# Kernel optimization log

Hardware: AMD Instinct MI355X
Metric: run time of the kernel (lower is better)

Reference implementation:

```python
import jax, jax.numpy as jnp
import numpy as np

NUM_SAMPLE = 10


def setup_inputs() -> dict:
    key = jax.random.key(0)
    k1, k2, k3, k4, k5 = jax.random.split(key, 5)
    N, F, B, S = 100000, 256, 20000, NUM_SAMPLE
    features_ue = jax.random.normal(k1, (N, F), dtype=jnp.float32)
    features_ap = jax.random.normal(k2, (N, F), dtype=jnp.float32)
    neigh_idx = jax.random.randint(k3, (B, S), 0, N, dtype=jnp.int32)
    nodes = jax.random.randint(k4, (B,), 0, N, dtype=jnp.int32)
    # xavier-uniform weight [embed_dim, feature_dim] = [256, 2*F]
    embed_dim, feature_dim = 256, 2 * F
    limit = float(np.sqrt(6.0 / (embed_dim + feature_dim)))
    weight = jax.random.uniform(k5, (embed_dim, feature_dim), dtype=jnp.float32,
                                minval=-limit, maxval=limit)
    return {"features_ue": features_ue, "features_ap": features_ap,
            "neigh_idx": neigh_idx, "nodes": nodes, "weight": weight}


def reference(features_ue, features_ap, neigh_idx, nodes, weight):
    # sample_model='ue2ue': other_feature = self_feature = features_ue
    S = neigh_idx.shape[1]
    # gather sampled neighbor features: [B, S, F] -> sum over S
    gathered = jnp.take(features_ue, neigh_idx, axis=0)
    # original: mask.div(num_neigh + 1), i.e. divide by count PLUS one
    neigh_feats = gathered.sum(axis=1) / jnp.float32(S + 1)  # [B, F]
    self_feats = jnp.take(features_ue, nodes, axis=0)        # [B, F]
    combined = jnp.concatenate([self_feats, neigh_feats], axis=1)  # [B, 2F]
    # weight.mm(combined.t()) then relu -> [embed_dim, B]
    out = jax.nn.relu(jnp.einsum('ef,bf->eb', weight, combined))
    return out
```

## Files before the change

kernel.cpp:

```cpp
#include <hip/hip_runtime.h>

typedef __attribute__((ext_vector_type(8))) short short8;
typedef __attribute__((ext_vector_type(4))) float f32x4;

#define B_TOTAL 20000
#define B_PAD   20096
#define NF      256
#define K2      512
#define NS      10

__device__ __forceinline__ unsigned short f2bf(float x) {
    unsigned u = __builtin_bit_cast(unsigned, x);
    u += 0x7FFFu + ((u >> 16) & 1u);
    return (unsigned short)(u >> 16);
}

__global__ __launch_bounds__(256) void gather_combine(
    const float* __restrict__ ue, const int* __restrict__ nidx,
    const int* __restrict__ nodes, const float* __restrict__ w,
    unsigned short* __restrict__ comb, unsigned short* __restrict__ wbf)
{
    const int t = threadIdx.x, blk = blockIdx.x;
    if (blk < 128) {
        const int base = blk * 1024 + t * 4;
        const float4 v = *(const float4*)(w + base);
        ushort4 o;
        o.x = f2bf(v.x); o.y = f2bf(v.y); o.z = f2bf(v.z); o.w = f2bf(v.w);
        *(ushort4*)(wbf + base) = o;
    }
    const int lane = t & 63;
    const int b = blk * 4 + (t >> 6);
    if (b >= B_PAD) return;
    unsigned short* crow = comb + (size_t)b * K2;
    if (b < B_TOTAL) {
        const int node = nodes[b];
        const float4 sf = ((const float4*)(ue + (size_t)node * NF))[lane];
        int myidx = 0;
        if (lane < NS) myidx = nidx[b * NS + lane];
        float ax = 0.f, ay = 0.f, az = 0.f, aw = 0.f;
        #pragma unroll
        for (int s = 0; s < NS; ++s) {
            const int is = __shfl(myidx, s);
            const float4 v = ((const float4*)(ue + (size_t)is * NF))[lane];
            ax += v.x; ay += v.y; az += v.z; aw += v.w;
        }
        const float inv = 1.0f / 11.0f;
        ushort4 s4, n4;
        s4.x = f2bf(sf.x); s4.y = f2bf(sf.y); s4.z = f2bf(sf.z); s4.w = f2bf(sf.w);
        n4.x = f2bf(ax * inv); n4.y = f2bf(ay * inv);
        n4.z = f2bf(az * inv); n4.w = f2bf(aw * inv);
        *(ushort4*)(crow + lane * 4) = s4;
        *(ushort4*)(crow + NF + lane * 4) = n4;
    } else {
        ushort4 z; z.x = z.y = z.z = z.w = 0;
        *(ushort4*)(crow + lane * 4) = z;
        *(ushort4*)(crow + NF + lane * 4) = z;
    }
}

__global__ __launch_bounds__(256) void gemm_relu(
    const unsigned short* __restrict__ wbf,
    const unsigned short* __restrict__ comb,
    float* __restrict__ out)
{
    __shared__ unsigned short Alds[8192];
    __shared__ unsigned short Blds[2048];
    const int t    = threadIdx.x;
    const int lane = t & 63;
    const int wv   = t >> 6;
    const int n0   = blockIdx.x * 32;
    const int m0   = blockIdx.y * 128;
    const int fr   = lane & 15;
    const int kq   = lane >> 4;

    f32x4 acc[2][2] = {};
    const short8* A8 = (const short8*)Alds;
    const short8* B8 = (const short8*)Blds;

    for (int ks = 0; ks < 8; ++ks) {
        #pragma unroll
        for (int L = 0; L < 4; ++L) {
            const int d16 = L * 256 + t;
            const int g = d16 >> 7, row = d16 & 127;
            const unsigned short* src = wbf + (size_t)(m0 + row) * K2 + ks * 64 + g * 8;
            __builtin_amdgcn_global_load_lds(
                (const __attribute__((address_space(1))) void*)src,
                (__attribute__((address_space(3))) void*)(Alds + (size_t)d16 * 8), 16, 0, 0);
        }
        {
            const int g = t >> 5, row = t & 31;
            const unsigned short* src = comb + (size_t)(n0 + row) * K2 + ks * 64 + g * 8;
            __builtin_amdgcn_global_load_lds(
                (const __attribute__((address_space(1))) void*)src,
                (__attribute__((address_space(3))) void*)(Blds + (size_t)t * 8), 16, 0, 0);
        }
        asm volatile("s_waitcnt vmcnt(0)" ::: "memory");
        __syncthreads();

        #pragma unroll
        for (int h = 0; h < 2; ++h) {
            short8 af[2], bg[2];
            #pragma unroll
            for (int i = 0; i < 2; ++i)
                af[i] = A8[(h * 4 + kq) * 128 + wv * 32 + i * 16 + fr];
            #pragma unroll
            for (int j = 0; j < 2; ++j)
                bg[j] = B8[(h * 4 + kq) * 32 + j * 16 + fr];
            #pragma unroll
            for (int i = 0; i < 2; ++i)
                #pragma unroll
                for (int j = 0; j < 2; ++j)
                    acc[i][j] = __builtin_amdgcn_mfma_f32_16x16x32_bf16(af[i], bg[j], acc[i][j], 0, 0, 0);
        }
        __syncthreads();
    }

    #pragma unroll
    for (int i = 0; i < 2; ++i) {
        const int e = m0 + wv * 32 + i * 16 + kq * 4;
        #pragma unroll
        for (int j = 0; j < 2; ++j) {
            const int b = n0 + j * 16 + fr;
            if (b < B_TOTAL) {
                #pragma unroll
                for (int r = 0; r < 4; ++r)
                    out[(size_t)(e + r) * B_TOTAL + b] = fmaxf(acc[i][j][r], 0.0f);
            }
        }
    }
}

extern "C" void kernel_launch(void* const* d_in, const int* in_sizes, int n_in,
                              void* d_out, int out_size, void* d_ws, size_t ws_size,
                              hipStream_t stream) {
    const float* ue    = (const float*)d_in[0];
    const int*   nidx  = (const int*)d_in[2];
    const int*   nodes = (const int*)d_in[3];
    const float* w     = (const float*)d_in[4];
    float*       out   = (float*)d_out;

    unsigned short* comb = (unsigned short*)d_ws;
    unsigned short* wbf  = comb + (size_t)B_PAD * K2;

    hipLaunchKernelGGL(gather_combine, dim3(B_PAD / 4), dim3(256), 0, stream,
                       ue, nidx, nodes, w, comb, wbf);
    hipLaunchKernelGGL(gemm_relu, dim3(B_PAD / 32, 2), dim3(256), 0, stream,
                       wbf, comb, out);
}
```

Before: 68.16 us.

## Double-buffer GEMM LDS tiles and widen N tile to 64

Restructures the bf16 MFMA GEMM so global-to-LDS loads for the next K-slice (now 32 wide) are issued while the current slice is being computed, using two LDS buffers. The per-block N tile grows from 32 to 64, so each block does 2x4 MFMA tiles per wave and half as many blocks launch. The goal is to hide load latency and reuse the weight tile across more columns. The explicit vmcnt wait is dropped, so correctness now relies on the compiler inserting the wait before the barrier. The gather kernel, which likely dominates runtime, is unchanged.

```diff
diff --git a/kernel.cpp b/kernel.cpp
--- a/kernel.cpp
+++ b/kernel.cpp
@@ -63,63 +63,74 @@
     const unsigned short* __restrict__ comb,
     float* __restrict__ out)
 {
-    __shared__ unsigned short Alds[8192];
-    __shared__ unsigned short Blds[2048];
+    __shared__ unsigned short Alds[2][4096];
+    __shared__ unsigned short Blds[2][2048];
     const int t    = threadIdx.x;
     const int lane = t & 63;
     const int wv   = t >> 6;
-    const int n0   = blockIdx.x * 32;
+    const int n0   = blockIdx.x * 64;
     const int m0   = blockIdx.y * 128;
     const int fr   = lane & 15;
     const int kq   = lane >> 4;
 
-    f32x4 acc[2][2] = {};
-    const short8* A8 = (const short8*)Alds;
-    const short8* B8 = (const short8*)Blds;
+    const int arow = t & 127, akg = t >> 7;
+    const int brow = t & 63,  bkg = t >> 6;
 
-    for (int ks = 0; ks < 8; ++ks) {
+    const unsigned short* gaBase = wbf  + (size_t)(m0 + arow) * K2 + akg * 8;
+    const unsigned short* gbBase = comb + (size_t)(n0 + brow) * K2 + bkg * 8;
+
+#define STAGE(nb, ks)                                                            \
+    do {                                                                         \
+        const unsigned short* ga = gaBase + (ks) * 32;                           \
+        const unsigned short* gb = gbBase + (ks) * 32;                           \
+        __builtin_amdgcn_global_load_lds(                                        \
+            (const __attribute__((address_space(1))) void*)ga,                   \
+            (__attribute__((address_space(3))) void*)(&Alds[nb][0] + t * 8),     \
+            16, 0, 0);                                                           \
+        __builtin_amdgcn_global_load_lds(                                        \
+            (const __attribute__((address_space(1))) void*)(ga + 16),            \
+            (__attribute__((address_space(3))) void*)(&Alds[nb][2048] + t * 8),  \
+            16, 0, 0);                                                           \
+        __builtin_amdgcn_global_load_lds(                                        \
+            (const __attribute__((address_space(1))) void*)gb,                   \
+            (__attribute__((address_space(3))) void*)(&Blds[nb][0] + t * 8),     \
+            16, 0, 0);                                                           \
+    } while (0)
+
+    f32x4 acc[2][4] = {};
+
+    STAGE(0, 0);
+    __syncthreads();
+
+    #pragma unroll
+    for (int ks = 0; ks < 16; ++ks) {
+        const int cur = ks & 1;
+        if (ks < 15) STAGE(cur ^ 1, ks + 1);
+
+        const short8* A8 = (const short8*)Alds[cur];
+        const short8* B8 = (const short8*)Blds[cur];
+        short8 af[2], bg[4];
         #pragma unroll
-        for (int L = 0; L < 4; ++L) {
-            const int d16 = L * 256 + t;
-            const int g = d16 >> 7, row = d16 & 127;
-            const unsigned short* src = wbf + (size_t)(m0 + row) * K2 + ks * 64 + g * 8;
-            __builtin_amdgcn_global_load_lds(
-                (const __attribute__((address_space(1))) void*)src,
-                (__attribute__((address_space(3))) void*)(Alds + (size_t)d16 * 8), 16, 0, 0);
-        }
-        {
-            const int g = t >> 5, row = t & 31;
-            const unsigned short* src = comb + (size_t)(n0 + row) * K2 + ks * 64 + g * 8;
-            __builtin_amdgcn_global_load_lds(
-                (const __attribute__((address_space(1))) void*)src,
-                (__attribute__((address_space(3))) void*)(Blds + (size_t)t * 8), 16, 0, 0);
-        }
-        asm volatile("s_waitcnt vmcnt(0)" ::: "memory");
-        __syncthreads();
+        for (int i = 0; i < 2; ++i)
+            af[i] = A8[kq * 128 + wv * 32 + i * 16 + fr];
+        #pragma unroll
+        for (int j = 0; j < 4; ++j)
+            bg[j] = B8[kq * 64 + j * 16 + fr];
+        #pragma unroll
+        for (int i = 0; i < 2; ++i)
+            #pragma unroll
+            for (int j = 0; j < 4; ++j)
+                acc[i][j] = __builtin_amdgcn_mfma_f32_16x16x32_bf16(af[i], bg[j], acc[i][j], 0, 0, 0);
 
-        #pragma unroll
-        for (int h = 0; h < 2; ++h) {
-            short8 af[2], bg[2];
-            #pragma unroll
-            for (int i = 0; i < 2; ++i)
-                af[i] = A8[(h * 4 + kq) * 128 + wv * 32 + i * 16 + fr];
-            #pragma unroll
-            for (int j = 0; j < 2; ++j)
-                bg[j] = B8[(h * 4 + kq) * 32 + j * 16 + fr];
-            #pragma unroll
-            for (int i = 0; i < 2; ++i)
-                #pragma unroll
-                for (int j = 0; j < 2; ++j)
-                    acc[i][j] = __builtin_amdgcn_mfma_f32_16x16x32_bf16(af[i], bg[j], acc[i][j], 0, 0, 0);
-        }
         __syncthreads();
     }
+#undef STAGE
 
     #pragma unroll
     for (int i = 0; i < 2; ++i) {
         const int e = m0 + wv * 32 + i * 16 + kq * 4;
         #pragma unroll
-        for (int j = 0; j < 2; ++j) {
+        for (int j = 0; j < 4; ++j) {
             const int b = n0 + j * 16 + fr;
             if (b < B_TOTAL) {
                 #pragma unroll
@@ -144,6 +155,6 @@
 
     hipLaunchKernelGGL(gather_combine, dim3(B_PAD / 4), dim3(256), 0, stream,
                        ue, nidx, nodes, w, comb, wbf);
-    hipLaunchKernelGGL(gemm_relu, dim3(B_PAD / 32, 2), dim3(256), 0, stream,
+    hipLaunchKernelGGL(gemm_relu, dim3(B_PAD / 64, 2), dim3(256), 0, stream,
                        wbf, comb, out);
 }
```

Result: faster. 61.55 us (-9.7%).
